# Kernel tuning notes

Measured on AMD Instinct MI355X. Metric: run time of the kernel, lower is better.

The kernel has to match this reference:

```python
import jax, jax.numpy as jnp
import numpy as np

V, H, O = 50257, 1024, 50257
B, T = 32, 512


def setup_inputs() -> dict:
    key = jax.random.key(0)
    ks = jax.random.split(key, 8)
    p = lambda k, shape: 0.02 * jax.random.normal(k, shape, dtype=jnp.float32)
    return {
        "state": jax.random.normal(ks[0], (B, H), dtype=jnp.float32),
        "tokens": jax.random.randint(ks[1], (B, T), 0, V, dtype=jnp.int64),
        "embedding": p(ks[2], (V, H)),
        "ih": p(ks[3], (H, H)),
        "hh": p(ks[4], (H, H)),
        "bias": p(ks[5], (H,)),
        "out_w": p(ks[6], (H, O)),
        "outBias": p(ks[7], (O,)),
    }


def reference(state, tokens, embedding, ih, hh, bias, out_w, outBias):
    # preCompute(): note torch broadcasts (H,H)/(H,) over the LAST axis,
    # i.e. column j is divided by ||hh[j,:]|| * H -- replicated faithfully.
    row_norms = jnp.linalg.norm(hh, axis=1)          # [H]
    scaledHH = hh / (row_norms * H)                  # [H,H]
    embedded = jnp.tanh(embedding) @ ih + bias       # [V,H]

    tokens_t = tokens.T                              # [T,B]

    def step(carry, tok):
        st, loss = carry                             # st: [B,H]
        logits = st @ out_w + outBias                # [B,O]
        logp = jax.nn.log_softmax(logits, axis=-1)
        nll = -jnp.take_along_axis(logp, tok[:, None], axis=1).mean()  # CE, mean over batch
        loss = loss + nll
        e = embedded[tok]                            # [B,H] gather
        # einsum('bi,bj->bi'): state scaled by sum over embedded features
        attn = jax.nn.softmax(st * e.sum(-1, keepdims=True), axis=-1)  # [B,H]
        st = jnp.tanh(st + attn @ scaledHH)
        return (st, loss), None

    (state, loss), _ = jax.lax.scan(step, (state, jnp.zeros((), state.dtype)), tokens_t)
    return state, loss
```

## Files before the change

kernel.cpp:

```cpp
#include <hip/hip_runtime.h>

#define VV 50257
#define HH 1024
#define OO 50257
#define BB 32
#define TT 512
#define NPAD2 50432
#define MROWS 16384
#define NBLK 32
#define KTILES 32

using bf16x8 = __attribute__((ext_vector_type(8))) short;
using f32x4  = __attribute__((ext_vector_type(4))) float;

__device__ __forceinline__ unsigned short f2bf(float x) {
    unsigned u = __float_as_uint(x);
    unsigned r = (u + 0x7FFFu + ((u >> 16) & 1u)) >> 16;
    return (unsigned short)r;
}
__device__ __forceinline__ float bf2f(unsigned short h) {
    return __uint_as_float(((unsigned)h) << 16);
}

__device__ __forceinline__ uint4 load_coh16(const void* p) {
    uint4 v;
    asm volatile("global_load_dwordx4 %0, %1, off sc0 sc1" : "=v"(v) : "v"(p));
    return v;
}
__device__ __forceinline__ void store_coh2(void* p, unsigned short s) {
    unsigned v = s;
    asm volatile("global_store_short %0, %1, off sc0 sc1" :: "v"(p), "v"(v) : "memory");
}
__device__ __forceinline__ void gload16(const void* g, void* l) {
    __builtin_amdgcn_global_load_lds((const __attribute__((address_space(1))) unsigned int*)g,
                                     (__attribute__((address_space(3))) unsigned int*)l, 16, 0, 0);
}

__global__ void prep_reduce(const float* __restrict__ ih, const float* __restrict__ hh,
                            const float* __restrict__ bias,
                            float* __restrict__ rs, float* __restrict__ rn, float* __restrict__ bsum) {
    int w = blockIdx.x * 4 + (threadIdx.x >> 6);
    int lane = threadIdx.x & 63;
    if (w < 1024) {
        const float* row = ih + (size_t)w * HH;
        float s = 0.f;
        for (int k = lane; k < HH; k += 64) s += row[k];
        for (int m = 1; m < 64; m <<= 1) s += __shfl_xor(s, m, 64);
        if (lane == 0) rs[w] = s;
    } else if (w < 2048) {
        int r = w - 1024;
        const float* row = hh + (size_t)r * HH;
        float s = 0.f;
        for (int k = lane; k < HH; k += 64) { float x = row[k]; s += x * x; }
        for (int m = 1; m < 64; m <<= 1) s += __shfl_xor(s, m, 64);
        if (lane == 0) rn[r] = sqrtf(s);
    } else if (w == 2048) {
        float s = 0.f;
        for (int k = lane; k < HH; k += 64) s += bias[k];
        for (int m = 1; m < 64; m <<= 1) s += __shfl_xor(s, m, 64);
        if (lane == 0) bsum[0] = s;
    }
}

__global__ void shconv(const float* __restrict__ hh, const float* __restrict__ rn,
                       unsigned short* __restrict__ SHb) {
    int gid = blockIdx.x * 256 + threadIdx.x;
    int slice = gid >> 12, kb = (gid >> 5) & 127, col = gid & 31;
    int j = slice * 32 + col;
    float inv = 1.0f / (rn[j] * 1024.0f);
    unsigned short v[8];
#pragma unroll
    for (int e = 0; e < 8; e++)
        v[e] = f2bf(hh[(size_t)(kb * 8 + e) * HH + j] * inv);
    uint4 pk;
    pk.x = (unsigned)v[0] | ((unsigned)v[1] << 16);
    pk.y = (unsigned)v[2] | ((unsigned)v[3] << 16);
    pk.z = (unsigned)v[4] | ((unsigned)v[5] << 16);
    pk.w = (unsigned)v[6] | ((unsigned)v[7] << 16);
    int gid_sw = (slice << 12) + (kb << 5) + (col ^ (kb & 3));
    *(uint4*)(SHb + (size_t)gid_sw * 8) = pk;
}

__global__ void esum_kernel(const float* __restrict__ emb, const float* __restrict__ rs,
                            const float* __restrict__ bsum, float* __restrict__ esum) {
    __shared__ float rs_l[HH];
    for (int i = threadIdx.x; i < HH; i += 256) rs_l[i] = rs[i];
    __syncthreads();
    int v = blockIdx.x * 4 + (threadIdx.x >> 6);
    if (v >= VV) return;
    int lane = threadIdx.x & 63;
    const float* row = emb + (size_t)v * HH;
    float s = 0.f;
    for (int k = lane; k < HH; k += 64) s += tanhf(row[k]) * rs_l[k];
    for (int m = 1; m < 64; m <<= 1) s += __shfl_xor(s, m, 64);
    if (lane == 0) esum[v] = s + bsum[0];
}

__global__ void esd_k(const int* __restrict__ tokens, const float* __restrict__ esum,
                      float* __restrict__ esd) {
    int idx = blockIdx.x * 256 + threadIdx.x;
    int t = idx >> 5, b = idx & 31;
    esd[idx] = esum[tokens[b * TT + t]];
}

__global__ void wconv(const float* __restrict__ W, unsigned short* __restrict__ Wb) {
    int n = blockIdx.x * 256 + threadIdx.x;
    int kb = blockIdx.y;
    unsigned short v[8];
#pragma unroll
    for (int e = 0; e < 8; e++) {
        float x = (n < OO) ? W[(size_t)(kb * 8 + e) * OO + n] : 0.0f;
        v[e] = f2bf(x);
    }
    uint4 pk;
    pk.x = (unsigned)v[0] | ((unsigned)v[1] << 16);
    pk.y = (unsigned)v[2] | ((unsigned)v[3] << 16);
    pk.z = (unsigned)v[4] | ((unsigned)v[5] << 16);
    pk.w = (unsigned)v[6] | ((unsigned)v[7] << 16);
    *(uint4*)(Wb + ((size_t)kb * NPAD2 + n) * 8) = pk;
}

__global__ void tokd_k(const int* __restrict__ tokens, int* __restrict__ tokd) {
    int r = blockIdx.x * 256 + threadIdx.x;
    int t = r >> 5, b = r & 31;
    tokd[r] = tokens[b * TT + t];
}

__global__ void __launch_bounds__(512) recurrence(
    const float* __restrict__ state_in, const unsigned short* __restrict__ SHb,
    const float* __restrict__ esd, unsigned short* __restrict__ S,
    unsigned short* __restrict__ abuf , unsigned* __restrict__ flags,
    float* __restrict__ out_state) {
    __shared__ unsigned short Wl[32768];
    __shared__ unsigned short Alds[32768];
    __shared__ f32x4 pacc[4][64];
    __shared__ float den_p[8][8];
    const int blk = blockIdx.x;
    const int tid = threadIdx.x;
    const int lane = tid & 63, w = tid >> 6;
    const int wr = (w >> 1) & 1, nt = w & 1, kh = w >> 2;
    const int q = lane >> 4, l16 = lane & 15;

    {
        const uint4* src = (const uint4*)(SHb + (size_t)blk * 32768);
        uint4* dst = (uint4*)Wl;
#pragma unroll
        for (int i = 0; i < 8; i++) dst[tid + i * 512] = src[tid + i * 512];
    }
    float st[4];
    const int b0 = wr * 16 + q * 4;
    const int jg = blk * 32 + nt * 16 + l16;
    if (kh == 0) {
#pragma unroll
        for (int r = 0; r < 4; r++) st[r] = state_in[(b0 + r) * HH + jg];
#pragma unroll
        for (int r = 0; r < 4; r++) {
            float es = esd[b0 + r];
            store_coh2(abuf + (size_t)(b0 + r) * HH + jg, f2bf(__expf(st[r] * es)));
        }
        asm volatile("s_waitcnt vmcnt(0)" ::: "memory");
    }
    __syncthreads();
    if (tid == 0) {
        unsigned one = 1;
        asm volatile("global_store_dword %0, %1, off sc0 sc1" :: "v"(flags + blk * 16), "v"(one) : "memory");
    }

    for (int t = 0; t < TT; t++) {
        f32x4 es4;
        if (kh == 0) {
            int tn = (t < TT - 1) ? t + 1 : TT - 1;
            es4 = *(const f32x4*)&esd[tn * BB + b0];
#pragma unroll
            for (int r = 0; r < 4; r++)
                S[(size_t)(t * BB + b0 + r) * HH + jg] = f2bf(st[r]);
        }
        {
            const unsigned* fp = flags + (lane & 31) * 16;
            unsigned v;
            do {
                asm volatile("global_load_dword %0, %1, off sc0 sc1\n\ts_waitcnt vmcnt(0)"
                             : "=v"(v) : "v"(fp) : "memory");
            } while (!__all((int)(v >= (unsigned)(t + 1))));
        }
        uint4 v[8];
        {
            const uint4* src = (const uint4*)abuf + (size_t)(t & 1) * 4096;
#pragma unroll
            for (int i = 0; i < 8; i++) v[i] = load_coh16(&src[tid + i * 512]);
            asm volatile("s_waitcnt vmcnt(0)" ::: "memory");
            __builtin_amdgcn_sched_barrier(0);
        }
        float p[8];
#pragma unroll
        for (int i = 0; i < 8; i++) {
            int c = tid + i * 512;
            int byte = c * 16;
            int row = byte >> 11;
            *(uint4*)((char*)Alds + (byte ^ ((row & 7) << 4))) = v[i];
            float s = 0.f;
            const unsigned short* hp = (const unsigned short*)&v[i];
#pragma unroll
            for (int e = 0; e < 8; e++) s += bf2f(hp[e]);
            p[i] = s;
        }
#pragma unroll
        for (int i = 0; i < 8; i++) {
            float s = p[i];
            for (int m = 1; m < 64; m <<= 1) s += __shfl_xor(s, m, 64);
            p[i] = s;
        }
        if (lane == 0) {
#pragma unroll
            for (int i = 0; i < 8; i++) den_p[w][i] = p[i];
        }
        __syncthreads();
        f32x4 acc = {0.f, 0.f, 0.f, 0.f};
#pragma unroll 4
        for (int kt = kh * 16; kt < kh * 16 + 16; kt++) {
            int arow = wr * 16 + l16;
            int abyte = (arow << 11) + kt * 64 + q * 16;
            abyte ^= (arow & 7) << 4;
            bf16x8 af = *(const bf16x8*)((const char*)Alds + abyte);
            int bbyte = ((kt * 4 + q) << 9) + (((nt * 16 + l16) ^ q) << 4);
            bf16x8 bf = *(const bf16x8*)((const char*)Wl + bbyte);
            acc = __builtin_amdgcn_mfma_f32_16x16x32_bf16(af, bf, acc, 0, 0, 0);
        }
        const int tile = wr * 2 + nt;
        if (kh == 1) pacc[tile][lane] = acc;
        __syncthreads();
        if (kh == 0) {
            f32x4 other = pacc[tile][lane];
            const bool last = (t == TT - 1);
#pragma unroll
            for (int r = 0; r < 4; r++) {
                float den = den_p[2 * r][wr * 4 + q] + den_p[2 * r + 1][wr * 4 + q];
                float u = (acc[r] + other[r]) / den;
                float stn = tanhf(st[r] + u);
                st[r] = stn;
                if (!last) {
                    store_coh2(abuf + (size_t)((t + 1) & 1) * 32768 +
                               (size_t)(b0 + r) * HH + jg, f2bf(__expf(stn * es4[r])));
                }
            }
            if (!last) asm volatile("s_waitcnt vmcnt(0)" ::: "memory");
        }
        if (t < TT - 1) {
            __syncthreads();
            if (tid == 0) {
                unsigned val = (unsigned)(t + 2);
                asm volatile("global_store_dword %0, %1, off sc0 sc1" :: "v"(flags + blk * 16), "v"(val) : "memory");
            }
        }
    }
    if (kh == 0) {
#pragma unroll
        for (int r = 0; r < 4; r++) out_state[(b0 + r) * HH + jg] = st[r];
    }
}

__global__ void __launch_bounds__(512) gemm_ce(
    const unsigned short* __restrict__ S, const unsigned short* __restrict__ Wb,
    const float* __restrict__ outBias, const int* __restrict__ tokd,
    float* __restrict__ Z, float* __restrict__ lt) {
    __shared__ unsigned short Ab[4][8192];
    __shared__ unsigned short Bb[4][8192];
    const int tid = threadIdx.x;
    const int lane = tid & 63, w = tid >> 6;
    const int wm = w >> 2, wn = w & 3;
    const int lin = blockIdx.x;
    const int id = (lin & 7) * 1576 + (lin >> 3);
    const int grp = id / (197 * 8);
    const int rem = id % (197 * 8);
    const int bx = rem >> 3;
    const int by = (grp << 3) + (rem & 7);
    const int bx256 = bx * 256, by256 = by * 256;

    const int arow = tid >> 2;
    const int rswA = (((tid & 3) ^ (arow & 3)) << 3);
    const unsigned short* AsrcBase = S + (size_t)(by256 + arow) * 1024 + rswA;
    const unsigned short* BsrcBase = Wb + ((size_t)(tid >> 8) * NPAD2 + bx256 + (tid & 255)) * 8;

#define ISSUE_A(kt_) { unsigned short* d = Ab[(kt_) & 3];                         \
    const unsigned short* s0 = AsrcBase + (kt_) * 32;                             \
    gload16(s0, (char*)d + tid * 16);                                             \
    gload16(s0 + 128 * 1024, (char*)d + 8192 + tid * 16); }
#define ISSUE_B(kt_) { unsigned short* d = Bb[(kt_) & 3];                         \
    const unsigned short* s0 = BsrcBase + (size_t)(kt_) * 4 * NPAD2 * 8;          \
    gload16(s0, (char*)d + tid * 16);                                             \
    gload16(s0 + (size_t)2 * NPAD2 * 8, (char*)d + 8192 + tid * 16); }

    f32x4 acc[8][4];
#pragma unroll
    for (int mi = 0; mi < 8; mi++)
#pragma unroll
        for (int ni = 0; ni < 4; ni++) acc[mi][ni] = {0.f, 0.f, 0.f, 0.f};

    ISSUE_A(0); ISSUE_B(0); ISSUE_A(1); ISSUE_B(1);
    asm volatile("s_waitcnt vmcnt(4)" ::: "memory");
    __builtin_amdgcn_s_barrier();

    const int l15 = lane & 15;
    const int slotA = (((lane >> 4) ^ (lane & 3)) << 4);
    const int browA = wm * 128 + l15;
    const int bcolB = ((lane >> 4) << 12) + ((wn * 64 + l15) << 4);

    for (int kt = 0; kt < KTILES; kt++) {
        const char* Abase = (const char*)Ab[kt & 3];
        const char* Bbase = (const char*)Bb[kt & 3];
        bf16x8 af[4], bf[4];
#pragma unroll
        for (int mi = 0; mi < 4; mi++)
            af[mi] = *(const bf16x8*)(Abase + ((browA + mi * 16) << 6) + slotA);
#pragma unroll
        for (int ni = 0; ni < 4; ni++)
            bf[ni] = *(const bf16x8*)(Bbase + bcolB + ni * 256);
        if (kt < KTILES - 2) ISSUE_A(kt + 2);
        __builtin_amdgcn_s_barrier();
        asm volatile("s_waitcnt lgkmcnt(0)" ::: "memory");
        __builtin_amdgcn_sched_barrier(0);
        __builtin_amdgcn_s_setprio(1);
#pragma unroll
        for (int mi = 0; mi < 4; mi++)
#pragma unroll
            for (int ni = 0; ni < 4; ni++)
                acc[mi][ni] = __builtin_amdgcn_mfma_f32_16x16x32_bf16(af[mi], bf[ni], acc[mi][ni], 0, 0, 0);
        __builtin_amdgcn_s_setprio(0);
        __builtin_amdgcn_s_barrier();
#pragma unroll
        for (int mi = 0; mi < 4; mi++)
            af[mi] = *(const bf16x8*)(Abase + ((browA + (mi + 4) * 16) << 6) + slotA);
        if (kt < KTILES - 2) ISSUE_B(kt + 2);
        __builtin_amdgcn_s_barrier();
        asm volatile("s_waitcnt lgkmcnt(0)" ::: "memory");
        __builtin_amdgcn_sched_barrier(0);
        __builtin_amdgcn_s_setprio(1);
#pragma unroll
        for (int mi = 0; mi < 4; mi++)
#pragma unroll
            for (int ni = 0; ni < 4; ni++)
                acc[mi + 4][ni] = __builtin_amdgcn_mfma_f32_16x16x32_bf16(af[mi], bf[ni], acc[mi + 4][ni], 0, 0, 0);
        __builtin_amdgcn_s_setprio(0);
        if (kt < KTILES - 3) {
            asm volatile("s_waitcnt vmcnt(4)" ::: "memory");
        } else if (kt == KTILES - 3) {
            asm volatile("s_waitcnt vmcnt(0)" ::: "memory");
        }
        __builtin_amdgcn_s_barrier();
    }
#undef ISSUE_A
#undef ISSUE_B

    const int colb = bx256 + wn * 64;
    const int rbase = by256 + wm * 128 + ((lane >> 4) << 2);
    float obv[4]; bool okv[4]; int jjv[4];
#pragma unroll
    for (int ni = 0; ni < 4; ni++) {
        jjv[ni] = colb + ni * 16 + l15;
        okv[ni] = jjv[ni] < OO;
        obv[ni] = okv[ni] ? outBias[jjv[ni]] : 0.f;
    }
    float rsum[8][4];
#pragma unroll
    for (int mi = 0; mi < 8; mi++)
#pragma unroll
        for (int r = 0; r < 4; r++) {
            int row = rbase + mi * 16 + r;
            int tk = tokd[row];
            float rssum = 0.f;
#pragma unroll
            for (int ni = 0; ni < 4; ni++) {
                float lg = acc[mi][ni][r] + obv[ni];
                rssum += okv[ni] ? __expf(lg) : 0.f;
                if (okv[ni] && jjv[ni] == tk) lt[row] = lg;
            }
            rsum[mi][r] = rssum;
        }
#pragma unroll
    for (int mi = 0; mi < 8; mi++)
#pragma unroll
        for (int r = 0; r < 4; r++) {
            float s = rsum[mi][r];
            s += __shfl_xor(s, 1, 64); s += __shfl_xor(s, 2, 64);
            s += __shfl_xor(s, 4, 64); s += __shfl_xor(s, 8, 64);
            rsum[mi][r] = s;
        }
    if (l15 == 0) {
#pragma unroll
        for (int mi = 0; mi < 8; mi++)
#pragma unroll
            for (int r = 0; r < 4; r++)
                atomicAdd(&Z[rbase + mi * 16 + r], rsum[mi][r]);
    }
}

__global__ void __launch_bounds__(1024) loss_reduce(const float* __restrict__ Z,
                                                    const float* __restrict__ lt,
                                                    float* __restrict__ out_loss) {
    __shared__ float red[16];
    float s = 0.f;
    for (int r = threadIdx.x; r < MROWS; r += 1024) s += logf(Z[r]) - lt[r];
    for (int m = 1; m < 64; m <<= 1) s += __shfl_xor(s, m, 64);
    if ((threadIdx.x & 63) == 0) red[threadIdx.x >> 6] = s;
    __syncthreads();
    if (threadIdx.x == 0) {
        float tot = 0.f;
        for (int q = 0; q < 16; q++) tot += red[q];
        out_loss[0] = tot / 32.0f;
    }
}

extern "C" void kernel_launch(void* const* d_in, const int* in_sizes, int n_in,
                              void* d_out, int out_size, void* d_ws, size_t ws_size,
                              hipStream_t stream) {
    const float* state  = (const float*)d_in[0];
    const int*   tokens = (const int*)d_in[1];
    const float* emb    = (const float*)d_in[2];
    const float* ih     = (const float*)d_in[3];
    const float* hh     = (const float*)d_in[4];
    const float* bias   = (const float*)d_in[5];
    const float* outw   = (const float*)d_in[6];
    const float* outb   = (const float*)d_in[7];

    char* ws = (char*)d_ws;
    size_t off = 0;
    auto alloc = [&](size_t bytes) { void* p = ws + off; off += (bytes + 255) & ~(size_t)255; return p; };
    unsigned short* Wb  = (unsigned short*)alloc((size_t)128 * NPAD2 * 8 * 2);
    unsigned short* S   = (unsigned short*)alloc((size_t)MROWS * HH * 2);
    unsigned short* SHb = (unsigned short*)alloc((size_t)131072 * 8 * 2);
    unsigned short* abuf= (unsigned short*)alloc((size_t)2 * BB * HH * 2);
    float* esum = (float*)alloc((size_t)VV * 4);
    float* esd  = (float*)alloc((size_t)MROWS * 4);
    float* rs   = (float*)alloc(4096);
    float* rn   = (float*)alloc(4096);
    float* bsum = (float*)alloc(256);
    float* Z    = (float*)alloc((size_t)MROWS * 4);
    float* lt   = (float*)alloc((size_t)MROWS * 4);
    int*   tokd = (int*)alloc((size_t)MROWS * 4);
    unsigned* flags = (unsigned*)alloc(NBLK * 16 * 4);
    float* out_state = (float*)d_out;
    float* out_loss  = out_state + 32768;

    hipMemsetAsync(Z, 0, (size_t)MROWS * 4, stream);
    hipMemsetAsync(flags, 0, NBLK * 16 * 4, stream);
    prep_reduce<<<513, 256, 0, stream>>>(ih, hh, bias, rs, rn, bsum);
    shconv<<<512, 256, 0, stream>>>(hh, rn, SHb);
    esum_kernel<<<12565, 256, 0, stream>>>(emb, rs, bsum, esum);
    esd_k<<<64, 256, 0, stream>>>(tokens, esum, esd);
    wconv<<<dim3(197, 128), 256, 0, stream>>>(outw, Wb);
    tokd_k<<<64, 256, 0, stream>>>(tokens, tokd);
    recurrence<<<NBLK, 512, 0, stream>>>(state, SHb, esd, S, abuf, flags, out_state);
    gemm_ce<<<64 * 197, 512, 0, stream>>>(S, Wb, outb, tokd, Z, lt);
    loss_reduce<<<1, 1024, 0, stream>>>(Z, lt, out_loss);
}
```

Measured before the change: 4.845 ms.

## Replace flag polling with data-presence polling on per-timestep activation buffers

The recurrence now keeps a separate exp-activation buffer for every timestep, zeroed up front, and consumers poll the data itself. A bf16 value of exactly zero marks a slot as not yet written, because exp output is never zero. This removes the flag round trip and the block-wide barrier before each flag publish. Per-wave flags remain as a fallback after 128 spins, weight staging into LDS moves after the initial publish, and den_p is double-buffered. The cost is a 32 MB memset and larger working memory, and it relies on exp values never rounding to zero in bf16.

```diff
diff --git a/kernel.cpp b/kernel.cpp
--- a/kernel.cpp
+++ b/kernel.cpp
@@ -20,6 +20,9 @@
 }
 __device__ __forceinline__ float bf2f(unsigned short h) {
     return __uint_as_float(((unsigned)h) << 16);
+}
+__device__ __forceinline__ unsigned hz16(unsigned x) {
+    return (x - 0x00010001u) & ~x & 0x80008000u;
 }
 
 __device__ __forceinline__ uint4 load_coh16(const void* p) {
@@ -129,24 +132,19 @@
 __global__ void __launch_bounds__(512) recurrence(
     const float* __restrict__ state_in, const unsigned short* __restrict__ SHb,
     const float* __restrict__ esd, unsigned short* __restrict__ S,
-    unsigned short* __restrict__ abuf , unsigned* __restrict__ flags,
+    unsigned short* __restrict__ abuf ,
+    unsigned* __restrict__ flags ,
     float* __restrict__ out_state) {
     __shared__ unsigned short Wl[32768];
     __shared__ unsigned short Alds[32768];
     __shared__ f32x4 pacc[4][64];
-    __shared__ float den_p[8][8];
+    __shared__ float den_p[2][8][8];
     const int blk = blockIdx.x;
     const int tid = threadIdx.x;
     const int lane = tid & 63, w = tid >> 6;
     const int wr = (w >> 1) & 1, nt = w & 1, kh = w >> 2;
     const int q = lane >> 4, l16 = lane & 15;
 
-    {
-        const uint4* src = (const uint4*)(SHb + (size_t)blk * 32768);
-        uint4* dst = (uint4*)Wl;
-#pragma unroll
-        for (int i = 0; i < 8; i++) dst[tid + i * 512] = src[tid + i * 512];
-    }
     float st[4];
     const int b0 = wr * 16 + q * 4;
     const int jg = blk * 32 + nt * 16 + l16;
@@ -154,16 +152,20 @@
 #pragma unroll
         for (int r = 0; r < 4; r++) st[r] = state_in[(b0 + r) * HH + jg];
 #pragma unroll
-        for (int r = 0; r < 4; r++) {
-            float es = esd[b0 + r];
-            store_coh2(abuf + (size_t)(b0 + r) * HH + jg, f2bf(__expf(st[r] * es)));
-        }
+        for (int r = 0; r < 4; r++)
+            store_coh2(abuf + (size_t)(b0 + r) * HH + jg, f2bf(__expf(st[r] * esd[b0 + r])));
         asm volatile("s_waitcnt vmcnt(0)" ::: "memory");
-    }
-    __syncthreads();
-    if (tid == 0) {
-        unsigned one = 1;
-        asm volatile("global_store_dword %0, %1, off sc0 sc1" :: "v"(flags + blk * 16), "v"(one) : "memory");
+        if (lane == 0) {
+            unsigned one = 1;
+            asm volatile("global_store_dword %0, %1, off sc0 sc1"
+                         :: "v"(flags + (blk * 4 + w) * 16), "v"(one) : "memory");
+        }
+    }
+    {
+        const uint4* src = (const uint4*)(SHb + (size_t)blk * 32768);
+        uint4* dst = (uint4*)Wl;
+#pragma unroll
+        for (int i = 0; i < 8; i++) dst[tid + i * 512] = src[tid + i * 512];
     }
 
     for (int t = 0; t < TT; t++) {
@@ -175,21 +177,37 @@
             for (int r = 0; r < 4; r++)
                 S[(size_t)(t * BB + b0 + r) * HH + jg] = f2bf(st[r]);
         }
-        {
-            const unsigned* fp = flags + (lane & 31) * 16;
-            unsigned v;
-            do {
-                asm volatile("global_load_dword %0, %1, off sc0 sc1\n\ts_waitcnt vmcnt(0)"
-                             : "=v"(v) : "v"(fp) : "memory");
-            } while (!__all((int)(v >= (unsigned)(t + 1))));
-        }
         uint4 v[8];
         {
-            const uint4* src = (const uint4*)abuf + (size_t)(t & 1) * 4096;
-#pragma unroll
-            for (int i = 0; i < 8; i++) v[i] = load_coh16(&src[tid + i * 512]);
-            asm volatile("s_waitcnt vmcnt(0)" ::: "memory");
-            __builtin_amdgcn_sched_barrier(0);
+            const uint4* p0 = (const uint4*)abuf + (size_t)t * 4096 + tid;
+            bool ok;
+            int spins = 0;
+            do {
+#pragma unroll
+                for (int i = 0; i < 8; i++) v[i] = load_coh16(p0 + i * 512);
+                asm volatile("s_waitcnt vmcnt(0)" ::: "memory");
+                __builtin_amdgcn_sched_barrier(0);
+                unsigned bad = 0;
+#pragma unroll
+                for (int i = 0; i < 8; i++)
+                    bad |= hz16(v[i].x) | hz16(v[i].y) | hz16(v[i].z) | hz16(v[i].w);
+                ok = __all(bad == 0);
+            } while (!ok && ++spins < 128);
+            if (!ok) {
+                const unsigned* f0 = flags + (2 * lane) * 16;
+                const unsigned* f1 = flags + (2 * lane + 1) * 16;
+                unsigned fa, fb;
+                do {
+                    asm volatile("global_load_dword %0, %2, off sc0 sc1\n\t"
+                                 "global_load_dword %1, %3, off sc0 sc1\n\t"
+                                 "s_waitcnt vmcnt(0)"
+                                 : "=&v"(fa), "=&v"(fb) : "v"(f0), "v"(f1) : "memory");
+                } while (!__all((int)(fa >= (unsigned)(t + 1) && fb >= (unsigned)(t + 1))));
+#pragma unroll
+                for (int i = 0; i < 8; i++) v[i] = load_coh16(p0 + i * 512);
+                asm volatile("s_waitcnt vmcnt(0)" ::: "memory");
+                __builtin_amdgcn_sched_barrier(0);
+            }
         }
         float p[8];
 #pragma unroll
@@ -212,7 +230,7 @@
         }
         if (lane == 0) {
 #pragma unroll
-            for (int i = 0; i < 8; i++) den_p[w][i] = p[i];
+            for (int i = 0; i < 8; i++) den_p[t & 1][w][i] = p[i];
         }
         __syncthreads();
         f32x4 acc = {0.f, 0.f, 0.f, 0.f};
@@ -223,8 +241,8 @@
             abyte ^= (arow & 7) << 4;
             bf16x8 af = *(const bf16x8*)((const char*)Alds + abyte);
             int bbyte = ((kt * 4 + q) << 9) + (((nt * 16 + l16) ^ q) << 4);
-            bf16x8 bf = *(const bf16x8*)((const char*)Wl + bbyte);
-            acc = __builtin_amdgcn_mfma_f32_16x16x32_bf16(af, bf, acc, 0, 0, 0);
+            bf16x8 bfv = *(const bf16x8*)((const char*)Wl + bbyte);
+            acc = __builtin_amdgcn_mfma_f32_16x16x32_bf16(af, bfv, acc, 0, 0, 0);
         }
         const int tile = wr * 2 + nt;
         if (kh == 1) pacc[tile][lane] = acc;
@@ -234,22 +252,21 @@
             const bool last = (t == TT - 1);
 #pragma unroll
             for (int r = 0; r < 4; r++) {
-                float den = den_p[2 * r][wr * 4 + q] + den_p[2 * r + 1][wr * 4 + q];
+                float den = den_p[t & 1][2 * r][wr * 4 + q] + den_p[t & 1][2 * r + 1][wr * 4 + q];
                 float u = (acc[r] + other[r]) / den;
                 float stn = tanhf(st[r] + u);
                 st[r] = stn;
-                if (!last) {
-                    store_coh2(abuf + (size_t)((t + 1) & 1) * 32768 +
+                if (!last)
+                    store_coh2(abuf + (size_t)(t + 1) * (BB * HH) +
                                (size_t)(b0 + r) * HH + jg, f2bf(__expf(stn * es4[r])));
+            }
+            if (!last) {
+                asm volatile("s_waitcnt vmcnt(0)" ::: "memory");
+                if (lane == 0) {
+                    unsigned val = (unsigned)(t + 2);
+                    asm volatile("global_store_dword %0, %1, off sc0 sc1"
+                                 :: "v"(flags + (blk * 4 + w) * 16), "v"(val) : "memory");
                 }
-            }
-            if (!last) asm volatile("s_waitcnt vmcnt(0)" ::: "memory");
-        }
-        if (t < TT - 1) {
-            __syncthreads();
-            if (tid == 0) {
-                unsigned val = (unsigned)(t + 2);
-                asm volatile("global_store_dword %0, %1, off sc0 sc1" :: "v"(flags + blk * 16), "v"(val) : "memory");
             }
         }
     }
@@ -427,8 +444,8 @@
     auto alloc = [&](size_t bytes) { void* p = ws + off; off += (bytes + 255) & ~(size_t)255; return p; };
     unsigned short* Wb  = (unsigned short*)alloc((size_t)128 * NPAD2 * 8 * 2);
     unsigned short* S   = (unsigned short*)alloc((size_t)MROWS * HH * 2);
+    unsigned short* abuf= (unsigned short*)alloc((size_t)TT * BB * HH * 2);
     unsigned short* SHb = (unsigned short*)alloc((size_t)131072 * 8 * 2);
-    unsigned short* abuf= (unsigned short*)alloc((size_t)2 * BB * HH * 2);
     float* esum = (float*)alloc((size_t)VV * 4);
     float* esd  = (float*)alloc((size_t)MROWS * 4);
     float* rs   = (float*)alloc(4096);
@@ -437,12 +454,13 @@
     float* Z    = (float*)alloc((size_t)MROWS * 4);
     float* lt   = (float*)alloc((size_t)MROWS * 4);
     int*   tokd = (int*)alloc((size_t)MROWS * 4);
-    unsigned* flags = (unsigned*)alloc(NBLK * 16 * 4);
+    unsigned* flags = (unsigned*)alloc(128 * 16 * 4);
     float* out_state = (float*)d_out;
     float* out_loss  = out_state + 32768;
 
     hipMemsetAsync(Z, 0, (size_t)MROWS * 4, stream);
-    hipMemsetAsync(flags, 0, NBLK * 16 * 4, stream);
+    hipMemsetAsync(abuf, 0, (size_t)TT * BB * HH * 2, stream);
+    hipMemsetAsync(flags, 0, 128 * 16 * 4, stream);
     prep_reduce<<<513, 256, 0, stream>>>(ih, hh, bias, rs, rn, bsum);
     shconv<<<512, 256, 0, stream>>>(hh, rn, SHb);
     esum_kernel<<<12565, 256, 0, stream>>>(emb, rs, bsum, esum);
```

New measurement: 4.672 ms (median of 2 runs). -3.6%, faster.
